# Kernel optimization log

Hardware: AMD Instinct MI355X
Metric: run time of the kernel (lower is better)

## Reference

```python
import jax, jax.numpy as jnp
import numpy as np
import math

CODE_DIMS = [32, 32]
NUM_CODEBOOK = 16
FEAT_DIM = 1024
EPS = 1e-12


def rms_norm(x, eps=EPS):
    var = jnp.mean(x * x, axis=-1, keepdims=True) + eps
    return x * jax.lax.rsqrt(var)


def outer_product(y, code_dims):
    # y: [..., h, sum(code_dims)] -> [..., h, prod(code_dims)]
    splits = list(np.cumsum(code_dims)[:-1])
    mats = jnp.split(y, splits, axis=-1)
    out = mats[0]
    for m in mats[1:]:
        out = out[..., :, None] * m[..., None, :]
        out = out.reshape(*out.shape[:-2], -1)
    return out


def setup_inputs() -> dict:
    key = jax.random.key(0)
    kx, kw = jax.random.split(key)
    x = jax.random.normal(kx, (4, 2048, FEAT_DIM), dtype=jnp.float32)
    std = math.sqrt(2.0 / (FEAT_DIM + sum(CODE_DIMS)))
    weight = jax.random.normal(kw, (NUM_CODEBOOK, FEAT_DIM, sum(CODE_DIMS)), dtype=jnp.float32) * std
    return {"x": x, "weight": weight}


def reference(x, weight):
    h = weight.shape[0]
    # batched per-codebook linear: [..., d] x [h, d, o] -> [..., h, o]
    y = jnp.einsum('...i,hio->...ho', x, weight)
    # chunked outer product per codebook -> [..., h, prod(code_dims)]
    op = outer_product(y, CODE_DIMS)
    out = jnp.mean(op, axis=-2) * math.sqrt(h)
    return rms_norm(out)
```

## Files before the change

### kernel.cpp

```cpp
#include <hip/hip_runtime.h>
#include <hip/hip_bf16.h>

#define KDIM  1024
#define NOUT  1024
#define NTOK  8192
#define NCB   16
#define BM    256
#define BN    128
#define BK    64
#define TILEB 49152
#define NBUF  3

typedef __attribute__((ext_vector_type(8))) short short8;
typedef __attribute__((ext_vector_type(4))) float f32x4;

__device__ static inline unsigned short f2bf(float f) {
    unsigned int u = __float_as_uint(f);
    return (unsigned short)((u + 0x7FFFu + ((u >> 16) & 1u)) >> 16);
}

__device__ static inline float bf2f(unsigned int h) {
    return __uint_as_float(h << 16);
}

__device__ static inline void async_copy16(const void* g, void* l) {
    __builtin_amdgcn_global_load_lds(
        (const __attribute__((address_space(1))) void*)g,
        (__attribute__((address_space(3))) void*)l, 16, 0, 0);
}

__global__ __launch_bounds__(256) void conv_kernel(const float* __restrict__ x,
                                                   const float* __restrict__ W,
                                                   unsigned short* __restrict__ A,
                                                   unsigned short* __restrict__ Bt) {
    int b = blockIdx.x;
    if (b < 4096) {
        int bb = (b & 7) * 512 + (b >> 3);
        int u = bb * 256 + threadIdx.x;
        const float* src = x + (size_t)u * 8;
        float4 v0 = *(const float4*)(src);
        float4 v1 = *(const float4*)(src + 4);
        short8 o;
        o[0] = (short)f2bf(v0.x); o[1] = (short)f2bf(v0.y);
        o[2] = (short)f2bf(v0.z); o[3] = (short)f2bf(v0.w);
        o[4] = (short)f2bf(v1.x); o[5] = (short)f2bf(v1.y);
        o[6] = (short)f2bf(v1.z); o[7] = (short)f2bf(v1.w);
        *(short8*)(A + (size_t)u * 8) = o;
    } else {
        int u = (b - 4096) * 256 + threadIdx.x;
        int n  = u & (NOUT - 1);
        int k0 = (u >> 10) << 3;
        int h = n >> 6, o = n & 63;
        const float* src = W + (size_t)h * KDIM * 64 + o;
        short8 v;
#pragma unroll
        for (int j = 0; j < 8; ++j)
            v[j] = (short)f2bf(src[(size_t)(k0 + j) * 64]);
        *(short8*)(Bt + (size_t)n * KDIM + k0) = v;
    }
}


__device__ __forceinline__ void stage_half(const unsigned short* __restrict__ A,
                                           const unsigned short* __restrict__ Bt,
                                           char* lbase, int tid, int m0, int n0,
                                           int kel, int half) {
    unsigned short* Als = (unsigned short*)lbase;
    unsigned short* Bls = (unsigned short*)(lbase + 32768);
#pragma unroll
    for (int i = 0; i < 2; ++i) {
        int s = (half * 2 + i) * 512 + tid;
        int row = s >> 3;
        int cs = (s & 7) ^ (row & 7);
        async_copy16(A + (size_t)(m0 + row) * KDIM + kel + cs * 8, Als + s * 8);
    }
    {
        int s = half * 512 + tid;
        int row = s >> 3;
        int cs = (s & 7) ^ (row & 7);
        async_copy16(Bt + (size_t)(n0 + row) * KDIM + kel + cs * 8, Bls + s * 8);
    }
}

__device__ __forceinline__ void read_frags(const char* lds, int buf, int chunk,
                                           int wm, int wn, int r15, int q,
                                           short8 (&af)[4], short8 (&bf)[4]) {
    const unsigned short* Al = (const unsigned short*)(lds + buf * TILEB);
    const unsigned short* Bl = Al + 16384;
#pragma unroll
    for (int mf = 0; mf < 4; ++mf) {
        int row = wm * 64 + mf * 16 + r15;
        af[mf] = *(const short8*)(Al + row * 64 + (((chunk + q) ^ (row & 7)) << 3));
    }
#pragma unroll
    for (int nf = 0; nf < 4; ++nf) {
        int row = wn * 64 + nf * 16 + r15;
        bf[nf] = *(const short8*)(Bl + row * 64 + (((chunk + q) ^ (row & 7)) << 3));
    }
}

__device__ __forceinline__ void mfma16(short8 (&af)[4], short8 (&bf)[4], f32x4 (&acc)[4][4]) {
    __builtin_amdgcn_s_setprio(1);
#pragma unroll
    for (int mf = 0; mf < 4; ++mf)
#pragma unroll
        for (int nf = 0; nf < 4; ++nf)
            acc[mf][nf] = __builtin_amdgcn_mfma_f32_16x16x32_bf16(af[mf], bf[nf], acc[mf][nf], 0, 0, 0);
    __builtin_amdgcn_s_setprio(0);
}

template <int VM, bool STAGE>
__device__ __forceinline__ void phase0(const unsigned short* __restrict__ A,
                                       const unsigned short* __restrict__ Bt,
                                       char* lds, int tid, int m0, int n0, int kt,
                                       int wm, int wn, int r15, int q,
                                       short8 (&afc)[4], short8 (&bfc)[4],
                                       short8 (&afn)[4], short8 (&bfn)[4],
                                       f32x4 (&acc)[4][4]) {
    asm volatile("s_waitcnt vmcnt(%0)" :: "i"(VM) : "memory");
    __builtin_amdgcn_sched_barrier(0);
    __builtin_amdgcn_s_barrier();
    __builtin_amdgcn_sched_barrier(0);
    if (STAGE)
        stage_half(A, Bt, lds + ((kt + 2) % NBUF) * TILEB, tid, m0, n0, (kt + 2) * BK, 0);
    read_frags(lds, kt % NBUF, 4, wm, wn, r15, q, afn, bfn);
    asm volatile("s_waitcnt lgkmcnt(8)" ::: "memory");
    __builtin_amdgcn_sched_barrier(0);
    mfma16(afc, bfc, acc);
}

template <int VM, bool STAGE, bool PRE>
__device__ __forceinline__ void phase1(const unsigned short* __restrict__ A,
                                       const unsigned short* __restrict__ Bt,
                                       char* lds, int tid, int m0, int n0, int kt,
                                       int wm, int wn, int r15, int q,
                                       short8 (&afc)[4], short8 (&bfc)[4],
                                       short8 (&afn)[4], short8 (&bfn)[4],
                                       f32x4 (&acc)[4][4]) {
    asm volatile("s_waitcnt vmcnt(%0)" :: "i"(VM) : "memory");
    __builtin_amdgcn_sched_barrier(0);
    __builtin_amdgcn_s_barrier();
    __builtin_amdgcn_sched_barrier(0);
    if (STAGE)
        stage_half(A, Bt, lds + ((kt + 2) % NBUF) * TILEB, tid, m0, n0, (kt + 2) * BK, 1);
    if (PRE) {
        read_frags(lds, (kt + 1) % NBUF, 0, wm, wn, r15, q, afn, bfn);
        asm volatile("s_waitcnt lgkmcnt(8)" ::: "memory");
    } else {
        asm volatile("s_waitcnt lgkmcnt(0)" ::: "memory");
    }
    __builtin_amdgcn_sched_barrier(0);
    mfma16(afc, bfc, acc);
}

__global__ __launch_bounds__(512, 2) void gemm_kernel(const unsigned short* __restrict__ A,
                                                      const unsigned short* __restrict__ Bt,
                                                      unsigned short* __restrict__ Y) {
    extern __shared__ char lds[];

    const int id  = blockIdx.x;
    const int xcd = id & 7;
    const int j   = id >> 3;
    const int m0  = (xcd * 4 + (j >> 3)) * BM;
    const int n0  = (j & 7) * BN;

    const int tid  = threadIdx.x;
    const int lane = tid & 63;
    const int w    = tid >> 6;
    const int wm   = w >> 1;
    const int wn   = w & 1;
    const int r15  = lane & 15;
    const int q    = lane >> 4;

    f32x4 acc[4][4];
#pragma unroll
    for (int mf = 0; mf < 4; ++mf)
#pragma unroll
        for (int nf = 0; nf < 4; ++nf)
            acc[mf][nf] = (f32x4){0.f, 0.f, 0.f, 0.f};

    short8 aF0[4], bF0[4], aF1[4], bF1[4];

    stage_half(A, Bt, lds,         tid, m0, n0, 0,  0);
    stage_half(A, Bt, lds,         tid, m0, n0, 0,  1);
    stage_half(A, Bt, lds + TILEB, tid, m0, n0, BK, 0);
    stage_half(A, Bt, lds + TILEB, tid, m0, n0, BK, 1);
    asm volatile("s_waitcnt vmcnt(6)" ::: "memory");
    __builtin_amdgcn_sched_barrier(0);
    __builtin_amdgcn_s_barrier();
    read_frags(lds, 0, 0, wm, wn, r15, q, aF0, bF0);

#pragma unroll 1
    for (int kt = 0; kt < 14; ++kt) {
        phase0<6, true>   (A, Bt, lds, tid, m0, n0, kt, wm, wn, r15, q, aF0, bF0, aF1, bF1, acc);
        phase1<3, true, true>(A, Bt, lds, tid, m0, n0, kt, wm, wn, r15, q, aF1, bF1, aF0, bF0, acc);
    }
    phase0<6, false>       (A, Bt, lds, tid, m0, n0, 14, wm, wn, r15, q, aF0, bF0, aF1, bF1, acc);
    phase1<0, false, true> (A, Bt, lds, tid, m0, n0, 14, wm, wn, r15, q, aF1, bF1, aF0, bF0, acc);
    phase0<0, false>       (A, Bt, lds, tid, m0, n0, 15, wm, wn, r15, q, aF0, bF0, aF1, bF1, acc);
    phase1<0, false, false>(A, Bt, lds, tid, m0, n0, 15, wm, wn, r15, q, aF1, bF1, aF0, bF0, acc);

#pragma unroll
    for (int mf = 0; mf < 4; ++mf)
#pragma unroll
        for (int nf = 0; nf < 4; ++nf) {
            int col = n0 + wn * 64 + nf * 16 + r15;
#pragma unroll
            for (int r = 0; r < 4; ++r) {
                int row = m0 + wm * 64 + mf * 16 + q * 4 + r;
                Y[(size_t)row * NOUT + col] = f2bf(acc[mf][nf][r]);
            }
        }
}

__global__ __launch_bounds__(256) void epilogue_kernel(const unsigned short* __restrict__ Y,
                                                       float* __restrict__ out) {
    __shared__ float ylds[1024];
    __shared__ float red[4];

    const int t = (blockIdx.x & 7) * 1024 + (blockIdx.x >> 3);
    const int tid = threadIdx.x;
    const unsigned short* yrow = Y + (size_t)t * NOUT;

    {
        uint2 raw = *(const uint2*)(yrow + tid * 4);
        ylds[tid * 4 + 0] = bf2f(raw.x & 0xffffu);
        ylds[tid * 4 + 1] = bf2f(raw.x >> 16);
        ylds[tid * 4 + 2] = bf2f(raw.y & 0xffffu);
        ylds[tid * 4 + 3] = bf2f(raw.y >> 16);
    }
    __syncthreads();

    const int jj = tid >> 3;
    const int k0 = (tid & 7) * 4;

    float o0 = 0.f, o1 = 0.f, o2 = 0.f, o3 = 0.f;
#pragma unroll
    for (int h = 0; h < NCB; ++h) {
        float a = ylds[h * 64 + jj];
        float4 bb = *(const float4*)&ylds[h * 64 + 32 + k0];
        o0 += a * bb.x; o1 += a * bb.y; o2 += a * bb.z; o3 += a * bb.w;
    }
    o0 *= 0.25f; o1 *= 0.25f; o2 *= 0.25f; o3 *= 0.25f;

    float ss = o0 * o0 + o1 * o1 + o2 * o2 + o3 * o3;
#pragma unroll
    for (int off = 32; off >= 1; off >>= 1)
        ss += __shfl_xor(ss, off, 64);

    const int lane = tid & 63, wv = tid >> 6;
    if (lane == 0) red[wv] = ss;
    __syncthreads();
    float tot = red[0] + red[1] + red[2] + red[3];
    float scale = rsqrtf(tot * (1.0f / 1024.0f) + 1e-12f);

    float4 o;
    o.x = o0 * scale; o.y = o1 * scale; o.z = o2 * scale; o.w = o3 * scale;
    *(float4*)(out + (size_t)t * 1024 + tid * 4) = o;
}

extern "C" void kernel_launch(void* const* d_in, const int* in_sizes, int n_in,
                              void* d_out, int out_size, void* d_ws, size_t ws_size,
                              hipStream_t stream) {
    const float* x   = (const float*)d_in[0];
    const float* wgt = (const float*)d_in[1];
    float* out = (float*)d_out;

    unsigned short* A  = (unsigned short*)d_ws;
    unsigned short* Bt = (unsigned short*)((char*)d_ws + (16u << 20));
    unsigned short* Y  = (unsigned short*)((char*)d_ws + (18u << 20));

    (void)hipFuncSetAttribute((const void*)gemm_kernel,
                              hipFuncAttributeMaxDynamicSharedMemorySize, NBUF * TILEB);

    conv_kernel<<<4096 + 512, 256, 0, stream>>>(x, wgt, A, Bt);
    gemm_kernel<<<(NTOK / BM) * (NOUT / BN), 512, NBUF * TILEB, stream>>>(A, Bt, Y);
    epilogue_kernel<<<NTOK, 256, 0, stream>>>(Y, out);
}
```

Before: 47.59 us.

## Restructure GEMM main loop to one barrier per K-tile with full-tile staging

Replaces the two-phase-per-K-tile software pipeline, which staged half-tiles and prefetched register fragments across barriers, with a single phase per K-tile. Each phase reads both K-halves of fragments from LDS, issues the full next-next tile's async copies, then runs two MFMA groups. This halves the number of block barriers but drops the cross-phase register prefetch, so LDS read latency is now exposed at the start of each tile. The vmcnt thresholds are kept the same even though each stage now issues six copies instead of three, so a wait of 6 no longer clearly guarantees the current tile has landed.

```diff
diff --git a/kernel.cpp b/kernel.cpp
--- a/kernel.cpp
+++ b/kernel.cpp
@@ -61,21 +61,21 @@
 }
 
 
-__device__ __forceinline__ void stage_half(const unsigned short* __restrict__ A,
+__device__ __forceinline__ void stage_tile(const unsigned short* __restrict__ A,
                                            const unsigned short* __restrict__ Bt,
-                                           char* lbase, int tid, int m0, int n0,
-                                           int kel, int half) {
+                                           char* lbase, int tid, int m0, int n0, int kel) {
     unsigned short* Als = (unsigned short*)lbase;
     unsigned short* Bls = (unsigned short*)(lbase + 32768);
 #pragma unroll
-    for (int i = 0; i < 2; ++i) {
-        int s = (half * 2 + i) * 512 + tid;
+    for (int i = 0; i < 4; ++i) {
+        int s = i * 512 + tid;
         int row = s >> 3;
         int cs = (s & 7) ^ (row & 7);
         async_copy16(A + (size_t)(m0 + row) * KDIM + kel + cs * 8, Als + s * 8);
     }
-    {
-        int s = half * 512 + tid;
+#pragma unroll
+    for (int i = 0; i < 2; ++i) {
+        int s = i * 512 + tid;
         int row = s >> 3;
         int cs = (s & 7) ^ (row & 7);
         async_copy16(Bt + (size_t)(n0 + row) * KDIM + kel + cs * 8, Bls + s * 8);
@@ -110,47 +110,27 @@
 }
 
 template <int VM, bool STAGE>
-__device__ __forceinline__ void phase0(const unsigned short* __restrict__ A,
-                                       const unsigned short* __restrict__ Bt,
-                                       char* lds, int tid, int m0, int n0, int kt,
-                                       int wm, int wn, int r15, int q,
-                                       short8 (&afc)[4], short8 (&bfc)[4],
-                                       short8 (&afn)[4], short8 (&bfn)[4],
-                                       f32x4 (&acc)[4][4]) {
+__device__ __forceinline__ void ktile(const unsigned short* __restrict__ A,
+                                      const unsigned short* __restrict__ Bt,
+                                      char* lds, int tid, int m0, int n0, int kt,
+                                      int wm, int wn, int r15, int q,
+                                      short8 (&aH0)[4], short8 (&bH0)[4],
+                                      short8 (&aH1)[4], short8 (&bH1)[4],
+                                      f32x4 (&acc)[4][4]) {
     asm volatile("s_waitcnt vmcnt(%0)" :: "i"(VM) : "memory");
     __builtin_amdgcn_sched_barrier(0);
     __builtin_amdgcn_s_barrier();
     __builtin_amdgcn_sched_barrier(0);
+    read_frags(lds, kt % NBUF, 0, wm, wn, r15, q, aH0, bH0);
+    read_frags(lds, kt % NBUF, 4, wm, wn, r15, q, aH1, bH1);
     if (STAGE)
-        stage_half(A, Bt, lds + ((kt + 2) % NBUF) * TILEB, tid, m0, n0, (kt + 2) * BK, 0);
-    read_frags(lds, kt % NBUF, 4, wm, wn, r15, q, afn, bfn);
+        stage_tile(A, Bt, lds + ((kt + 2) % NBUF) * TILEB, tid, m0, n0, (kt + 2) * BK);
     asm volatile("s_waitcnt lgkmcnt(8)" ::: "memory");
     __builtin_amdgcn_sched_barrier(0);
-    mfma16(afc, bfc, acc);
-}
-
-template <int VM, bool STAGE, bool PRE>
-__device__ __forceinline__ void phase1(const unsigned short* __restrict__ A,
-                                       const unsigned short* __restrict__ Bt,
-                                       char* lds, int tid, int m0, int n0, int kt,
-                                       int wm, int wn, int r15, int q,
-                                       short8 (&afc)[4], short8 (&bfc)[4],
-                                       short8 (&afn)[4], short8 (&bfn)[4],
-                                       f32x4 (&acc)[4][4]) {
-    asm volatile("s_waitcnt vmcnt(%0)" :: "i"(VM) : "memory");
-    __builtin_amdgcn_sched_barrier(0);
-    __builtin_amdgcn_s_barrier();
-    __builtin_amdgcn_sched_barrier(0);
-    if (STAGE)
-        stage_half(A, Bt, lds + ((kt + 2) % NBUF) * TILEB, tid, m0, n0, (kt + 2) * BK, 1);
-    if (PRE) {
-        read_frags(lds, (kt + 1) % NBUF, 0, wm, wn, r15, q, afn, bfn);
-        asm volatile("s_waitcnt lgkmcnt(8)" ::: "memory");
-    } else {
-        asm volatile("s_waitcnt lgkmcnt(0)" ::: "memory");
-    }
-    __builtin_amdgcn_sched_barrier(0);
-    mfma16(afc, bfc, acc);
+    mfma16(aH0, bH0, acc);
+    asm volatile("s_waitcnt lgkmcnt(0)" ::: "memory");
+    __builtin_amdgcn_sched_barrier(0);
+    mfma16(aH1, bH1, acc);
 }
 
 __global__ __launch_bounds__(512, 2) void gemm_kernel(const unsigned short* __restrict__ A,
@@ -179,26 +159,16 @@
         for (int nf = 0; nf < 4; ++nf)
             acc[mf][nf] = (f32x4){0.f, 0.f, 0.f, 0.f};
 
-    short8 aF0[4], bF0[4], aF1[4], bF1[4];
-
-    stage_half(A, Bt, lds,         tid, m0, n0, 0,  0);
-    stage_half(A, Bt, lds,         tid, m0, n0, 0,  1);
-    stage_half(A, Bt, lds + TILEB, tid, m0, n0, BK, 0);
-    stage_half(A, Bt, lds + TILEB, tid, m0, n0, BK, 1);
-    asm volatile("s_waitcnt vmcnt(6)" ::: "memory");
-    __builtin_amdgcn_sched_barrier(0);
-    __builtin_amdgcn_s_barrier();
-    read_frags(lds, 0, 0, wm, wn, r15, q, aF0, bF0);
+    short8 aH0[4], bH0[4], aH1[4], bH1[4];
+
+    stage_tile(A, Bt, lds,         tid, m0, n0, 0);
+    stage_tile(A, Bt, lds + TILEB, tid, m0, n0, BK);
 
 #pragma unroll 1
-    for (int kt = 0; kt < 14; ++kt) {
-        phase0<6, true>   (A, Bt, lds, tid, m0, n0, kt, wm, wn, r15, q, aF0, bF0, aF1, bF1, acc);
-        phase1<3, true, true>(A, Bt, lds, tid, m0, n0, kt, wm, wn, r15, q, aF1, bF1, aF0, bF0, acc);
-    }
-    phase0<6, false>       (A, Bt, lds, tid, m0, n0, 14, wm, wn, r15, q, aF0, bF0, aF1, bF1, acc);
-    phase1<0, false, true> (A, Bt, lds, tid, m0, n0, 14, wm, wn, r15, q, aF1, bF1, aF0, bF0, acc);
-    phase0<0, false>       (A, Bt, lds, tid, m0, n0, 15, wm, wn, r15, q, aF0, bF0, aF1, bF1, acc);
-    phase1<0, false, false>(A, Bt, lds, tid, m0, n0, 15, wm, wn, r15, q, aF1, bF1, aF0, bF0, acc);
+    for (int kt = 0; kt < 14; ++kt)
+        ktile<6, true>(A, Bt, lds, tid, m0, n0, kt, wm, wn, r15, q, aH0, bH0, aH1, bH1, acc);
+    ktile<6, false>(A, Bt, lds, tid, m0, n0, 14, wm, wn, r15, q, aH0, bH0, aH1, bH1, acc);
+    ktile<0, false>(A, Bt, lds, tid, m0, n0, 15, wm, wn, r15, q, aH0, bH0, aH1, bH1, acc);
 
 #pragma unroll
     for (int mf = 0; mf < 4; ++mf)
```

After: 46.64 us (median of 2 runs). 2.0% less time.
